# Optimization experiments

Hardware: AMD Instinct MI355X
Metric: run time of the kernel (lower is better)

Reference implementation:

```python
import jax, jax.numpy as jnp
import numpy as np

NUM_CLASSES = 80
NUM_ANCHORS = 3
STRIDES = (8, 16, 32)
FMP_SIZES = ((160, 160), (80, 80), (40, 40))  # 1280x1280 input
TOPK = 1000
CONF_THRESH = 0.01
NMS_THRESH = 0.5

ANCHOR_SIZE_VALS = np.array([[[12, 16], [19, 36], [40, 28]],
                             [[36, 75], [76, 55], [72, 146]],
                             [[142, 110], [192, 243], [459, 401]]], dtype=np.float32)


def setup_inputs() -> dict:
    key = jax.random.key(0)
    ks = jax.random.split(key, 9)
    inp = {}
    for lvl, (h, w) in enumerate(FMP_SIZES):
        m = h * w * NUM_ANCHORS
        inp[f"obj{lvl}"] = jax.random.normal(ks[3 * lvl + 0], (m, 1), dtype=jnp.float32)
        inp[f"cls{lvl}"] = jax.random.normal(ks[3 * lvl + 1], (m, NUM_CLASSES), dtype=jnp.float32)
        inp[f"reg{lvl}"] = jax.random.normal(ks[3 * lvl + 2], (m, 4), dtype=jnp.float32)
    inp["anchor_size"] = jnp.asarray(ANCHOR_SIZE_VALS)
    return inp


def _generate_anchors(fmp_h, fmp_w, anchor_wh):
    # anchor_wh: [A, 2] in pixels. Returns [H*W*A, 4] = (cx_cell+0.5, cy_cell+0.5, w, h)
    ys, xs = jnp.meshgrid(jnp.arange(fmp_h), jnp.arange(fmp_w), indexing="ij")
    xy = jnp.stack([xs, ys], axis=-1).astype(jnp.float32).reshape(-1, 1, 2) + 0.5
    xy = jnp.broadcast_to(xy, (fmp_h * fmp_w, NUM_ANCHORS, 2)).reshape(-1, 2)
    wh = jnp.broadcast_to(anchor_wh[None, :, :], (fmp_h * fmp_w, NUM_ANCHORS, 2)).reshape(-1, 2)
    return jnp.concatenate([xy, wh], axis=-1)


def _decode_boxes(reg, anchors, stride):
    # ctr = (sigmoid(txy)*3 - 1.5 + grid_xy) * stride ; wh = exp(twh) * anchor_wh
    ctr = (jax.nn.sigmoid(reg[:, :2]) * 3.0 - 1.5 + anchors[:, :2]) * stride
    wh = jnp.exp(reg[:, 2:]) * anchors[:, 2:]
    return jnp.concatenate([ctr - 0.5 * wh, ctr + 0.5 * wh], axis=-1)  # [M,4] x1y1x2y2


def _pairwise_iou(b):
    x1 = jnp.maximum(b[:, None, 0], b[None, :, 0])
    y1 = jnp.maximum(b[:, None, 1], b[None, :, 1])
    x2 = jnp.minimum(b[:, None, 2], b[None, :, 2])
    y2 = jnp.minimum(b[:, None, 3], b[None, :, 3])
    inter = jnp.clip(x2 - x1, 0.0) * jnp.clip(y2 - y1, 0.0)
    area = (b[:, 2] - b[:, 0]) * (b[:, 3] - b[:, 1])
    union = area[:, None] + area[None, :] - inter
    return inter / jnp.maximum(union, 1e-9)


def _postprocess(objs, clss, regs, anchor_size):
    all_scores, all_labels, all_boxes, all_valid = [], [], [], []
    for lvl in range(3):
        h, w = FMP_SIZES[lvl]
        anchors = _generate_anchors(h, w, anchor_size[lvl])
        boxes = _decode_boxes(regs[lvl], anchors, float(STRIDES[lvl]))  # [M,4]
        # multi-label score: sqrt(sigmoid(obj) * sigmoid(cls)), flattened over [M*C]
        scores_flat = jnp.sqrt(jax.nn.sigmoid(objs[lvl]) * jax.nn.sigmoid(clss[lvl])).reshape(-1)
        vals, idxs = jax.lax.top_k(scores_flat, TOPK)
        anchor_idx = idxs // NUM_CLASSES
        labels = idxs % NUM_CLASSES
        all_scores.append(vals)
        all_labels.append(labels)
        all_boxes.append(boxes[anchor_idx])
        all_valid.append(vals > CONF_THRESH)
    scores = jnp.concatenate(all_scores)   # [3*TOPK]
    labels = jnp.concatenate(all_labels)
    boxes = jnp.concatenate(all_boxes)     # [3*TOPK, 4]
    valid = jnp.concatenate(all_valid)

    K = scores.shape[0]
    order = jnp.argsort(-jnp.where(valid, scores, -1.0))
    scores_s = scores[order]
    labels_s = labels[order]
    boxes_s = boxes[order]
    valid_s = valid[order]

    # class-aware NMS: offset boxes by label so different classes never overlap
    off_scale = jnp.max(boxes_s) + 1.0
    boxes_off = boxes_s + (labels_s.astype(jnp.float32) * off_scale)[:, None]
    iou = _pairwise_iou(boxes_off)  # [K,K]
    idx_range = jnp.arange(K)

    def body(i, keep):
        sup = keep[i] & (iou[i] > NMS_THRESH) & (idx_range > i)
        return keep & (~sup)

    keep = jax.lax.fori_loop(0, K, body, valid_s)
    return boxes_s, scores_s * keep.astype(scores_s.dtype), labels_s, keep


def reference(obj0, cls0, reg0, obj1, cls1, reg1, obj2, cls2, reg2, anchor_size):
    return _postprocess((obj0, obj1, obj2), (cls0, cls1, cls2), (reg0, reg1, reg2), anchor_size)
```

## Files before the change

kernel.cpp:

```cpp
#include <hip/hip_runtime.h>
#include <math.h>
#include <float.h>

#define NC 80
#define TOPKN 1000
#define K3 3000
#define NB 5120
#define BASE 0x3F333333u
#define CANDT 0x3F4CCCCDu
#define CAP 4096
#define NWORD 48
#define MROWS 3136
#define MC0 6144000
#define MC1 1536000
#define MC2 384000
#define NQ 2016000u
#define QL0 1536000u
#define QL01 1920000u
#define BQ 2048u
#define CCAP0 262144
#define CCAP1 65536
#define CCAP2 16384

__device__ __forceinline__ float sigf(float x) { return 1.0f / (1.0f + expf(-x)); }

__global__ void k_init(unsigned* candCnt) {
    if (threadIdx.x < 3) candCnt[threadIdx.x] = 0u;
}

__global__ __launch_bounds__(256) void k_pass1(
        const float* __restrict__ obj0, const float* __restrict__ cls0,
        const float* __restrict__ obj1, const float* __restrict__ cls1,
        const float* __restrict__ obj2, const float* __restrict__ cls2,
        unsigned* __restrict__ candCnt,
        unsigned long long* __restrict__ cand0,
        unsigned long long* __restrict__ cand1,
        unsigned long long* __restrict__ cand2) {
    __shared__ unsigned lcnt[3], lbase[3], lwr[3];
    int tid = threadIdx.x;
    if (tid < 3) { lcnt[tid] = 0u; lwr[tid] = 0u; }
    __syncthreads();
    unsigned qbase = blockIdx.x * BQ;
    unsigned mask32 = 0u;
    for (int it = 0; it < 8; ++it) {
        unsigned q = qbase + (unsigned)it * 256u + (unsigned)tid;
        if (q >= NQ) continue;
        int lvl; unsigned q2; const float* obj; const float* cls;
        if (q < QL0)       { lvl = 0; q2 = q;         obj = obj0; cls = cls0; }
        else if (q < QL01) { lvl = 1; q2 = q - QL0;   obj = obj1; cls = cls1; }
        else               { lvl = 2; q2 = q - QL01;  obj = obj2; cls = cls2; }
        float so = sigf(obj[q2 / 20u]);
        float4 cv = ((const float4*)cls)[q2];
#define PA(J, C) { float s = sqrtf(so * sigf(C)); unsigned ub = __float_as_uint(s); \
        if (ub > CANDT) { mask32 |= (1u << (it * 4 + (J))); atomicAdd(&lcnt[lvl], 1u); } }
        PA(0, cv.x) PA(1, cv.y) PA(2, cv.z) PA(3, cv.w)
#undef PA
    }
    __syncthreads();
    if (tid < 3 && lcnt[tid] > 0u) lbase[tid] = atomicAdd(&candCnt[tid], lcnt[tid]);
    __syncthreads();
    if (mask32) {
        for (int it = 0; it < 8; ++it) {
            unsigned g = (mask32 >> (it * 4)) & 0xFu;
            if (!g) continue;
            unsigned q = qbase + (unsigned)it * 256u + (unsigned)tid;
            int lvl; unsigned q2; const float* obj; const float* cls;
            unsigned long long* cnd; unsigned ccap;
            if (q < QL0)       { lvl = 0; q2 = q;        obj = obj0; cls = cls0; cnd = cand0; ccap = CCAP0; }
            else if (q < QL01) { lvl = 1; q2 = q - QL0;  obj = obj1; cls = cls1; cnd = cand1; ccap = CCAP1; }
            else               { lvl = 2; q2 = q - QL01; obj = obj2; cls = cls2; cnd = cand2; ccap = CCAP2; }
            float so = sigf(obj[q2 / 20u]);
            float4 cv = ((const float4*)cls)[q2];
#define PB(J, C) if (g & (1u << (J))) { \
            float s = sqrtf(so * sigf(C)); unsigned ub = __float_as_uint(s); \
            unsigned pos = lbase[lvl] + atomicAdd(&lwr[lvl], 1u); \
            if (pos < ccap) cnd[pos] = ((unsigned long long)ub << 32) | (unsigned long long)(q2 * 4u + (J)); }
            PB(0, cv.x) PB(1, cv.y) PB(2, cv.z) PB(3, cv.w)
#undef PB
        }
    }
}

__device__ __forceinline__ bool before_desc(float sa, int ia, float sb, int ib) {
    return (sa > sb) || (sa == sb && ia < ib);
}

__global__ __launch_bounds__(1024) void k_topk(
    const float* __restrict__ reg0, const float* __restrict__ reg1, const float* __restrict__ reg2,
    const float* __restrict__ anchor_size,
    const unsigned* __restrict__ candCnt,
    const unsigned long long* __restrict__ cand0,
    const unsigned long long* __restrict__ cand1,
    const unsigned long long* __restrict__ cand2,
    float* __restrict__ scoresC, int* __restrict__ labelsC,
    unsigned* __restrict__ validC, float* __restrict__ boxesC) {
    __shared__ unsigned lh[NB];
    __shared__ unsigned part[1024];
    __shared__ float ss[CAP];
    __shared__ int   si[CAP];
    __shared__ int selS, fcntS;
    int lvl = blockIdx.x;
    int t = threadIdx.x;
    const unsigned long long* cand; unsigned ccap;
    if (lvl == 0)      { cand = cand0; ccap = CCAP0; }
    else if (lvl == 1) { cand = cand1; ccap = CCAP1; }
    else               { cand = cand2; ccap = CCAP2; }
    unsigned n = candCnt[lvl]; if (n > ccap) n = ccap;
    for (int i = t; i < NB; i += 1024) lh[i] = 0u;
    if (t == 0) fcntS = 0;
    __syncthreads();
    for (unsigned i = t; i < n; i += 1024) {
        unsigned ub = (unsigned)(cand[i] >> 32);
        unsigned b = (ub - BASE) >> 10; if (b >= NB) b = NB - 1;
        atomicAdd(&lh[b], 1u);
    }
    __syncthreads();
    unsigned ps = 0;
    for (int k = 0; k < 5; ++k) ps += lh[t * 5 + k];
    part[t] = ps;
    __syncthreads();
    if (t == 0) {
        unsigned cum = 0; int sel = 0;
        for (int c = 1023; c >= 0; --c) {
            if (cum + part[c] >= TOPKN) {
                int b0 = c * 5;
                for (int b = b0 + 4; b >= b0; --b) {
                    cum += lh[b];
                    if (cum >= TOPKN) { sel = b; break; }
                }
                break;
            }
            cum += part[c];
        }
        selS = sel;
    }
    __syncthreads();
    unsigned sel = (unsigned)selS;
    for (unsigned i = t; i < n; i += 1024) {
        unsigned long long pk = cand[i];
        unsigned ub = (unsigned)(pk >> 32);
        unsigned b = (ub - BASE) >> 10; if (b >= NB) b = NB - 1;
        if (b >= sel) {
            int pos = atomicAdd(&fcntS, 1);
            if (pos < CAP) { ss[pos] = __uint_as_float(ub); si[pos] = (int)(unsigned)(pk & 0xFFFFFFFFull); }
        }
    }
    __syncthreads();
    int n2 = fcntS; if (n2 > CAP) n2 = CAP;
    int P2 = (n2 > 2048) ? CAP : 2048;
    for (int i = t; i < P2; i += 1024)
        if (i >= n2) { ss[i] = -FLT_MAX; si[i] = 0x7FFFFFFF; }
    __syncthreads();
    for (int k = 2; k <= P2; k <<= 1) {
        for (int j = k >> 1; j > 0; j >>= 1) {
            for (int p = t; p < P2; p += 1024) {
                int l = p ^ j;
                if (l > p) {
                    float sp = ss[p], sl = ss[l]; int ip = si[p], il = si[l];
                    bool up = ((p & k) == 0);
                    if (before_desc(sp, ip, sl, il) != up) {
                        ss[p] = sl; ss[l] = sp; si[p] = il; si[l] = ip;
                    }
                }
            }
            __syncthreads();
        }
    }
    if (t < TOPKN) {
        int r = t;
        float v = ss[r]; int idx = si[r];
        int o = lvl * TOPKN + r;
        if (idx == 0x7FFFFFFF) {
            boxesC[o * 4 + 0] = 0.f; boxesC[o * 4 + 1] = 0.f;
            boxesC[o * 4 + 2] = 0.f; boxesC[o * 4 + 3] = 0.f;
            scoresC[o] = v; labelsC[o] = 0; validC[o] = 0u;
        } else {
            int m = idx / NC; int c = idx - m * NC;
            int cell = m / 3, a = m - cell * 3;
            int W; float st; const float* reg;
            if (lvl == 0)      { W = 160; st = 8.0f;  reg = reg0; }
            else if (lvl == 1) { W = 80;  st = 16.0f; reg = reg1; }
            else               { W = 40;  st = 32.0f; reg = reg2; }
            float ax = (float)(cell % W) + 0.5f;
            float ay = (float)(cell / W) + 0.5f;
            float tx = reg[m * 4 + 0], ty = reg[m * 4 + 1], tw = reg[m * 4 + 2], th = reg[m * 4 + 3];
            float cx = (sigf(tx) * 3.0f - 1.5f + ax) * st;
            float cy = (sigf(ty) * 3.0f - 1.5f + ay) * st;
            float aw = anchor_size[lvl * 6 + a * 2 + 0];
            float ah = anchor_size[lvl * 6 + a * 2 + 1];
            float w = expf(tw) * aw, h = expf(th) * ah;
            boxesC[o * 4 + 0] = cx - 0.5f * w;
            boxesC[o * 4 + 1] = cy - 0.5f * h;
            boxesC[o * 4 + 2] = cx + 0.5f * w;
            boxesC[o * 4 + 3] = cy + 0.5f * h;
            scoresC[o] = v;
            labelsC[o] = c;
            validC[o] = (v > 0.01f) ? 1u : 0u;
        }
    }
}

__global__ void k_max(const float* __restrict__ boxesC, float* __restrict__ off_scale) {
    float m = -FLT_MAX;
    for (int i = threadIdx.x; i < K3 * 4; i += 1024) m = fmaxf(m, boxesC[i]);
    for (int o = 32; o > 0; o >>= 1) m = fmaxf(m, __shfl_down(m, o, 64));
    __shared__ float p[16];
    if ((threadIdx.x & 63) == 0) p[threadIdx.x >> 6] = m;
    __syncthreads();
    if (threadIdx.x == 0) {
        float mm = p[0];
        for (int i = 1; i < 16; ++i) mm = fmaxf(mm, p[i]);
        *off_scale = mm + 1.0f;
    }
}

__global__ __launch_bounds__(1024) void k_sort(
    const float* __restrict__ scoresC, const int* __restrict__ labelsC,
    const unsigned* __restrict__ validC, const float* __restrict__ boxesC,
    float* __restrict__ scores_s, int* __restrict__ labels_s,
    unsigned* __restrict__ valid_s, float* __restrict__ boxes_s,
    float* __restrict__ dout) {
    const int P2 = 4096;
    __shared__ float ks[4096];
    __shared__ int   si[4096];
    int t = threadIdx.x;
    for (int i = t; i < P2; i += 1024) {
        if (i < K3) { ks[i] = validC[i] ? scoresC[i] : -1.0f; si[i] = i; }
        else        { ks[i] = -FLT_MAX;                        si[i] = 0x7FFFFFFF; }
    }
    __syncthreads();
    for (int k = 2; k <= P2; k <<= 1) {
        for (int j = k >> 1; j > 0; j >>= 1) {
            for (int p = t; p < P2; p += 1024) {
                int l = p ^ j;
                if (l > p) {
                    float sp = ks[p], sl = ks[l]; int ip = si[p], il = si[l];
                    bool up = ((p & k) == 0);
                    if (before_desc(sp, ip, sl, il) != up) {
                        ks[p] = sl; ks[l] = sp; si[p] = il; si[l] = ip;
                    }
                }
            }
            __syncthreads();
        }
    }
    for (int r = t; r < K3; r += 1024) {
        int o = si[r];
        float sc = scoresC[o];
        int lb = labelsC[o];
        scores_s[r] = sc;
        labels_s[r] = lb;
        valid_s[r] = validC[o];
        float b0 = boxesC[o * 4 + 0], b1 = boxesC[o * 4 + 1];
        float b2 = boxesC[o * 4 + 2], b3 = boxesC[o * 4 + 3];
        boxes_s[r * 4 + 0] = b0; boxes_s[r * 4 + 1] = b1;
        boxes_s[r * 4 + 2] = b2; boxes_s[r * 4 + 3] = b3;
        dout[r * 4 + 0] = b0; dout[r * 4 + 1] = b1;
        dout[r * 4 + 2] = b2; dout[r * 4 + 3] = b3;
        dout[15000 + r] = (float)lb;
    }
}

__global__ void k_mask(const float* __restrict__ boxes_s, const int* __restrict__ labels_s,
                       const float* __restrict__ off_scale,
                       unsigned long long* __restrict__ mask) {
    int i = blockIdx.x;
    int wv = threadIdx.x >> 6, lane = threadIdx.x & 63;
    int w = blockIdx.y * 4 + wv;
    int j = w * 64 + lane;
    float off = *off_scale;
    float oi = (float)labels_s[i] * off;
    float ai0 = boxes_s[i * 4 + 0] + oi, ai1 = boxes_s[i * 4 + 1] + oi;
    float ai2 = boxes_s[i * 4 + 2] + oi, ai3 = boxes_s[i * 4 + 3] + oi;
    bool p = false;
    if (j < K3 && j > i) {
        float oj = (float)labels_s[j] * off;
        float bj0 = boxes_s[j * 4 + 0] + oj, bj1 = boxes_s[j * 4 + 1] + oj;
        float bj2 = boxes_s[j * 4 + 2] + oj, bj3 = boxes_s[j * 4 + 3] + oj;
        float x1 = fmaxf(ai0, bj0), y1 = fmaxf(ai1, bj1);
        float x2 = fminf(ai2, bj2), y2 = fminf(ai3, bj3);
        float inter = fmaxf(x2 - x1, 0.0f) * fmaxf(y2 - y1, 0.0f);
        float areai = (ai2 - ai0) * (ai3 - ai1);
        float areaj = (bj2 - bj0) * (bj3 - bj1);
        float uni = areai + areaj - inter;
        float iou = inter / fmaxf(uni, 1e-9f);
        p = iou > 0.5f;
    }
    unsigned long long b = __ballot(p ? 1 : 0);
    if (lane == 0) mask[(size_t)i * NWORD + w] = b;
}

#define X24(M) M(0) M(1) M(2) M(3) M(4) M(5) M(6) M(7) M(8) M(9) M(10) M(11) \
               M(12) M(13) M(14) M(15) M(16) M(17) M(18) M(19) M(20) M(21) M(22) M(23)
#define X16P(M,SB) M(SB,0) M(SB,1) M(SB,2) M(SB,3) M(SB,4) M(SB,5) M(SB,6) M(SB,7) \
                   M(SB,8) M(SB,9) M(SB,10) M(SB,11) M(SB,12) M(SB,13) M(SB,14) M(SB,15)
#define DECLST(K) ulonglong2 st##K;
#define LOADM(K)  st##K = srcp[(K) * 64];
#define WRITEM(K) dstp[(K) * 64] = st##K;
#define RDM(SB,T) d##T = Bp[(SB) * 16 + (T)][w]; c##T = Bp[(SB) * 16 + (T)][lidx];
#define STEPM(SB,T) { unsigned long long _s = 0ull - ((cw >> ((SB) * 16 + (T))) & 1ull); \
                      cw &= ~(d##T & _s); kw &= ~(c##T & _s); }
#define SUBBLK(SB) { X16P(RDM, SB) X16P(STEPM, SB) }

__global__ __launch_bounds__(64, 1) void k_scan(
        const unsigned* __restrict__ valid_s,
        const unsigned long long* __restrict__ maskU,
        const float* __restrict__ scores_s,
        float* __restrict__ dout) {
    __shared__ __align__(16) unsigned long long buf[2][64][NWORD];
    int lane = threadIdx.x;
    int lidx = (lane < NWORD) ? lane : (NWORD - 1);
    unsigned long long kw = 0ull;
    for (int w = 0; w < 47; ++w) {
        int j = w * 64 + lane;
        unsigned long long b = __ballot((j < K3 && valid_s[j]) ? 1 : 0);
        if (lane == w) kw = b;
    }
    X24(DECLST)
    { const ulonglong2* srcp = ((const ulonglong2*)maskU) + lane;                      X24(LOADM) }
    { ulonglong2* dstp = ((ulonglong2*)&buf[0][0][0]) + lane;                          X24(WRITEM) }
    { const ulonglong2* srcp = ((const ulonglong2*)(maskU + 64 * NWORD)) + lane;       X24(LOADM) }
    const int NW = 47;
    for (int w = 0; w < NW; ++w) {
        { ulonglong2* dstp = ((ulonglong2*)&buf[(w + 1) & 1][0][0]) + lane;            X24(WRITEM) }
        { const ulonglong2* srcp = ((const ulonglong2*)(maskU + (size_t)(w + 2) * 64 * NWORD)) + lane; X24(LOADM) }
        unsigned long long cw = __shfl(kw, w, 64);
        unsigned long long (*Bp)[NWORD] = buf[w & 1];
        unsigned long long d0, d1, d2, d3, d4, d5, d6, d7, d8, d9, d10, d11, d12, d13, d14, d15;
        unsigned long long c0, c1, c2, c3, c4, c5, c6, c7, c8, c9, c10, c11, c12, c13, c14, c15;
        SUBBLK(0) SUBBLK(1) SUBBLK(2) SUBBLK(3)
    }
    __syncthreads();
    unsigned long long* sk = &buf[0][0][0];
    if (lane < 47) sk[lane] = kw;
    __syncthreads();
    for (int j = lane; j < K3; j += 64) {
        int b = (int)((sk[j >> 6] >> (j & 63)) & 1ull);
        dout[12000 + j] = b ? scores_s[j] : 0.0f;
        dout[18000 + j] = (float)b;
    }
}

extern "C" void kernel_launch(void* const* d_in, const int* in_sizes, int n_in,
                              void* d_out, int out_size, void* d_ws, size_t ws_size,
                              hipStream_t stream) {
    const float* obj0 = (const float*)d_in[0];
    const float* cls0 = (const float*)d_in[1];
    const float* reg0 = (const float*)d_in[2];
    const float* obj1 = (const float*)d_in[3];
    const float* cls1 = (const float*)d_in[4];
    const float* reg1 = (const float*)d_in[5];
    const float* obj2 = (const float*)d_in[6];
    const float* cls2 = (const float*)d_in[7];
    const float* reg2 = (const float*)d_in[8];
    const float* anc  = (const float*)d_in[9];

    char* p = (char*)d_ws;
    auto alloc = [&](size_t bytes, size_t align) -> void* {
        size_t a = (size_t)p; a = (a + align - 1) / align * align;
        p = (char*)a; void* r = (void*)p; p += bytes; return r;
    };
    unsigned* candCnt    = (unsigned*)alloc(16, 16);
    unsigned long long* cand0 = (unsigned long long*)alloc((size_t)CCAP0 * 8, 256);
    unsigned long long* cand1 = (unsigned long long*)alloc((size_t)CCAP1 * 8, 256);
    unsigned long long* cand2 = (unsigned long long*)alloc((size_t)CCAP2 * 8, 256);
    float*    scoresC    = (float*)alloc(K3 * 4, 16);
    int*      labelsC    = (int*)alloc(K3 * 4, 16);
    unsigned* validC     = (unsigned*)alloc(K3 * 4, 16);
    float*    boxesC     = (float*)alloc((size_t)K3 * 16, 16);
    float*    scores_s   = (float*)alloc(K3 * 4, 16);
    int*      labels_s   = (int*)alloc(K3 * 4, 16);
    unsigned* valid_s    = (unsigned*)alloc(K3 * 4, 16);
    float*    boxes_s    = (float*)alloc((size_t)K3 * 16, 16);
    float*    off_scale  = (float*)alloc(16, 16);
    unsigned long long* mask = (unsigned long long*)alloc((size_t)MROWS * NWORD * 8, 256);
    (void)ws_size; (void)in_sizes; (void)n_in; (void)out_size;

    k_init<<<1, 64, 0, stream>>>(candCnt);
    k_pass1<<<(NQ + BQ - 1) / BQ, 256, 0, stream>>>(obj0, cls0, obj1, cls1, obj2, cls2,
                                                    candCnt, cand0, cand1, cand2);
    k_topk<<<3, 1024, 0, stream>>>(reg0, reg1, reg2, anc, candCnt, cand0, cand1, cand2,
                                   scoresC, labelsC, validC, boxesC);
    k_max<<<1, 1024, 0, stream>>>(boxesC, off_scale);
    k_sort<<<1, 1024, 0, stream>>>(scoresC, labelsC, validC, boxesC,
                                   scores_s, labels_s, valid_s, boxes_s, (float*)d_out);
    k_mask<<<dim3(K3, 12), 256, 0, stream>>>(boxes_s, labels_s, off_scale, mask);
    k_scan<<<1, 64, 0, stream>>>(valid_s, mask, scores_s, (float*)d_out);
}
```

Baseline: 419.3 us.

## Use readlane broadcasts in NMS scan and loop mask chunks per block

The serial NMS scan kernel no longer reads the diagonal word through a separate per-lane LDS load. It now loads only each lane's own column word, broadcasts the diagonal word with readlane, and accumulates suppression into 32-bit halves that are applied once per block row. The goal is to shorten the single-wave serial critical path by halving LDS reads and using scalar broadcasts. The mask kernel also switches from a 2D grid to 3000 blocks that each loop over 12 chunks, which reuses the row box and hoists its area, but reduces the number of blocks in flight.

```diff
diff --git a/kernel.cpp b/kernel.cpp
--- a/kernel.cpp
+++ b/kernel.cpp
@@ -261,33 +261,36 @@
     }
 }
 
-__global__ void k_mask(const float* __restrict__ boxes_s, const int* __restrict__ labels_s,
-                       const float* __restrict__ off_scale,
-                       unsigned long long* __restrict__ mask) {
+__global__ __launch_bounds__(256) void k_mask(
+        const float* __restrict__ boxes_s, const int* __restrict__ labels_s,
+        const float* __restrict__ off_scale,
+        unsigned long long* __restrict__ mask) {
     int i = blockIdx.x;
     int wv = threadIdx.x >> 6, lane = threadIdx.x & 63;
-    int w = blockIdx.y * 4 + wv;
-    int j = w * 64 + lane;
     float off = *off_scale;
     float oi = (float)labels_s[i] * off;
     float ai0 = boxes_s[i * 4 + 0] + oi, ai1 = boxes_s[i * 4 + 1] + oi;
     float ai2 = boxes_s[i * 4 + 2] + oi, ai3 = boxes_s[i * 4 + 3] + oi;
-    bool p = false;
-    if (j < K3 && j > i) {
-        float oj = (float)labels_s[j] * off;
-        float bj0 = boxes_s[j * 4 + 0] + oj, bj1 = boxes_s[j * 4 + 1] + oj;
-        float bj2 = boxes_s[j * 4 + 2] + oj, bj3 = boxes_s[j * 4 + 3] + oj;
-        float x1 = fmaxf(ai0, bj0), y1 = fmaxf(ai1, bj1);
-        float x2 = fminf(ai2, bj2), y2 = fminf(ai3, bj3);
-        float inter = fmaxf(x2 - x1, 0.0f) * fmaxf(y2 - y1, 0.0f);
-        float areai = (ai2 - ai0) * (ai3 - ai1);
-        float areaj = (bj2 - bj0) * (bj3 - bj1);
-        float uni = areai + areaj - inter;
-        float iou = inter / fmaxf(uni, 1e-9f);
-        p = iou > 0.5f;
-    }
-    unsigned long long b = __ballot(p ? 1 : 0);
-    if (lane == 0) mask[(size_t)i * NWORD + w] = b;
+    float areai = (ai2 - ai0) * (ai3 - ai1);
+    for (int chunk = 0; chunk < 12; ++chunk) {
+        int w = chunk * 4 + wv;
+        int j = w * 64 + lane;
+        bool p = false;
+        if (j < K3 && j > i) {
+            float oj = (float)labels_s[j] * off;
+            float bj0 = boxes_s[j * 4 + 0] + oj, bj1 = boxes_s[j * 4 + 1] + oj;
+            float bj2 = boxes_s[j * 4 + 2] + oj, bj3 = boxes_s[j * 4 + 3] + oj;
+            float x1 = fmaxf(ai0, bj0), y1 = fmaxf(ai1, bj1);
+            float x2 = fminf(ai2, bj2), y2 = fminf(ai3, bj3);
+            float inter = fmaxf(x2 - x1, 0.0f) * fmaxf(y2 - y1, 0.0f);
+            float areaj = (bj2 - bj0) * (bj3 - bj1);
+            float uni = areai + areaj - inter;
+            float iou = inter / fmaxf(uni, 1e-9f);
+            p = iou > 0.5f;
+        }
+        unsigned long long b = __ballot(p ? 1 : 0);
+        if (lane == 0) mask[(size_t)i * NWORD + w] = b;
+    }
 }
 
 #define X24(M) M(0) M(1) M(2) M(3) M(4) M(5) M(6) M(7) M(8) M(9) M(10) M(11) \
@@ -297,10 +300,16 @@
 #define DECLST(K) ulonglong2 st##K;
 #define LOADM(K)  st##K = srcp[(K) * 64];
 #define WRITEM(K) dstp[(K) * 64] = st##K;
-#define RDM(SB,T) d##T = Bp[(SB) * 16 + (T)][w]; c##T = Bp[(SB) * 16 + (T)][lidx];
-#define STEPM(SB,T) { unsigned long long _s = 0ull - ((cw >> ((SB) * 16 + (T))) & 1ull); \
-                      cw &= ~(d##T & _s); kw &= ~(c##T & _s); }
-#define SUBBLK(SB) { X16P(RDM, SB) X16P(STEPM, SB) }
+#define LDC(SB,T) uint2 c##T = Bq[((SB) * 16 + (T)) * NWORD];
+#define STEPS(SB,T) { \
+    unsigned dlo = (unsigned)__builtin_amdgcn_readlane((int)c##T.x, w); \
+    unsigned dhi = (unsigned)__builtin_amdgcn_readlane((int)c##T.y, w); \
+    unsigned on = (unsigned)((cw >> ((SB) * 16 + (T))) & 1ull); \
+    unsigned long long d = (((unsigned long long)dhi) << 32) | (unsigned long long)dlo; \
+    cw &= ~(on ? d : 0ull); \
+    unsigned sm = on ? 0xFFFFFFFFu : 0u; \
+    slo |= c##T.x & sm; shi |= c##T.y & sm; }
+#define SUBBLK2(SB, SL, SH) { unsigned &slo = SL, &shi = SH; X16P(LDC, SB) X16P(STEPS, SB) }
 
 __global__ __launch_bounds__(64, 1) void k_scan(
         const unsigned* __restrict__ valid_s,
@@ -310,11 +319,11 @@
     __shared__ __align__(16) unsigned long long buf[2][64][NWORD];
     int lane = threadIdx.x;
     int lidx = (lane < NWORD) ? lane : (NWORD - 1);
-    unsigned long long kw = 0ull;
+    unsigned kwlo = 0u, kwhi = 0u;
     for (int w = 0; w < 47; ++w) {
         int j = w * 64 + lane;
         unsigned long long b = __ballot((j < K3 && valid_s[j]) ? 1 : 0);
-        if (lane == w) kw = b;
+        if (lane == w) { kwlo = (unsigned)b; kwhi = (unsigned)(b >> 32); }
     }
     X24(DECLST)
     { const ulonglong2* srcp = ((const ulonglong2*)maskU) + lane;                      X24(LOADM) }
@@ -324,15 +333,20 @@
     for (int w = 0; w < NW; ++w) {
         { ulonglong2* dstp = ((ulonglong2*)&buf[(w + 1) & 1][0][0]) + lane;            X24(WRITEM) }
         { const ulonglong2* srcp = ((const ulonglong2*)(maskU + (size_t)(w + 2) * 64 * NWORD)) + lane; X24(LOADM) }
-        unsigned long long cw = __shfl(kw, w, 64);
-        unsigned long long (*Bp)[NWORD] = buf[w & 1];
-        unsigned long long d0, d1, d2, d3, d4, d5, d6, d7, d8, d9, d10, d11, d12, d13, d14, d15;
-        unsigned long long c0, c1, c2, c3, c4, c5, c6, c7, c8, c9, c10, c11, c12, c13, c14, c15;
-        SUBBLK(0) SUBBLK(1) SUBBLK(2) SUBBLK(3)
+        unsigned long long cw =
+            (((unsigned long long)(unsigned)__builtin_amdgcn_readlane((int)kwhi, w)) << 32)
+          |  ((unsigned long long)(unsigned)__builtin_amdgcn_readlane((int)kwlo, w));
+        const uint2* Bq = ((const uint2*)&buf[w & 1][0][0]) + lidx;
+        unsigned s0l = 0u, s0h = 0u, s1l = 0u, s1h = 0u;
+        unsigned s2l = 0u, s2h = 0u, s3l = 0u, s3h = 0u;
+        SUBBLK2(0, s0l, s0h) SUBBLK2(1, s1l, s1h)
+        SUBBLK2(2, s2l, s2h) SUBBLK2(3, s3l, s3h)
+        kwlo &= ~(s0l | s1l | s2l | s3l);
+        kwhi &= ~(s0h | s1h | s2h | s3h);
     }
     __syncthreads();
     unsigned long long* sk = &buf[0][0][0];
-    if (lane < 47) sk[lane] = kw;
+    if (lane < 47) sk[lane] = (((unsigned long long)kwhi) << 32) | (unsigned long long)kwlo;
     __syncthreads();
     for (int j = lane; j < K3; j += 64) {
         int b = (int)((sk[j >> 6] >> (j & 63)) & 1ull);
@@ -384,6 +398,6 @@
     k_max<<<1, 1024, 0, stream>>>(boxesC, off_scale);
     k_sort<<<1, 1024, 0, stream>>>(scoresC, labelsC, validC, boxesC,
                                    scores_s, labels_s, valid_s, boxes_s, (float*)d_out);
-    k_mask<<<dim3(K3, 12), 256, 0, stream>>>(boxes_s, labels_s, off_scale, mask);
+    k_mask<<<K3, 256, 0, stream>>>(boxes_s, labels_s, off_scale, mask);
     k_scan<<<1, 64, 0, stream>>>(valid_s, mask, scores_s, (float*)d_out);
 }
```

Result: slower. 452.0 us (+7.8%).
